# Kernel optimization log

Measured on AMD Instinct MI355X. Metric: run time of the kernel, lower is better.

The kernel has to match this reference:

```python
import jax, jax.numpy as jnp
import numpy as np

DIM = 1024
HEADS = 16


def setup_inputs() -> dict:
    key = jax.random.key(0)
    k1, k2, k3, k4 = jax.random.split(key, 4)
    x = jax.random.normal(k1, (4, 2048, DIM), dtype=jnp.float32)
    # torch nn.Linear weights: [out_features, in_features]
    w_qkv = jax.random.normal(k2, (3 * DIM, DIM), dtype=jnp.float32) * (DIM ** -0.5)
    w_out = jax.random.normal(k3, (DIM, DIM), dtype=jnp.float32) * (DIM ** -0.5)
    b_out = jax.random.normal(k4, (DIM,), dtype=jnp.float32) * 0.01
    return {"x": x, "w_qkv": w_qkv, "w_out": w_out, "b_out": b_out}


def reference(x, w_qkv, w_out, b_out):
    b, n, d = x.shape
    h = HEADS
    hd = d // h
    scale = d ** -0.5  # note: full dim, matching the original module
    qkv = jnp.einsum('bnd,ed->bne', x, w_qkv)  # [b, n, 3d]
    q, k, v = jnp.split(qkv, 3, axis=-1)
    def to_heads(t):
        return t.reshape(b, n, h, hd).transpose(0, 2, 1, 3)  # [b, h, n, hd]
    q, k, v = map(to_heads, (q, k, v))
    dots = jnp.einsum('bhqd,bhkd->bhqk', q, k) * scale  # [b, h, n, n]
    attn = jax.nn.softmax(dots, axis=-1)
    out = jnp.einsum('bhqk,bhkd->bhqd', attn, v)  # [b, h, n, hd]
    out = out.transpose(0, 2, 1, 3).reshape(b, n, d)
    return jnp.einsum('bnd,ed->bne', out, w_out) + b_out
```

## Files before the change

kernel.cpp:

```cpp
#include <hip/hip_runtime.h>
#include <stdint.h>

#define SEQ   2048
#define NDIM  1024
#define NH    16
#define HD    64
#define KDIM  1024

typedef short  short8  __attribute__((ext_vector_type(8)));
typedef float  floatx4 __attribute__((ext_vector_type(4)));
typedef unsigned short ushort4v __attribute__((ext_vector_type(4)));
typedef _Float16 half4 __attribute__((ext_vector_type(4)));
typedef __fp16  fp16x2 __attribute__((ext_vector_type(2)));
typedef __fp16  fp16x4 __attribute__((ext_vector_type(4)));

typedef __attribute__((address_space(1))) void GV;
typedef __attribute__((address_space(3))) void LV;

#define QSCALE 0.04508422003f

__device__ __forceinline__ unsigned short f2bf(float f) {
    unsigned int u = __float_as_uint(f);
    u += 0x7fffu + ((u >> 16) & 1u);
    return (unsigned short)(u >> 16);
}

__global__ __launch_bounds__(256) void cast_f32_bf16(const float* __restrict__ in,
                                                     unsigned short* __restrict__ out) {
    int i = (blockIdx.x * 256 + threadIdx.x) * 4;
    float4 v = *(const float4*)(in + i);
    ushort4v o;
    o.x = f2bf(v.x); o.y = f2bf(v.y); o.z = f2bf(v.z); o.w = f2bf(v.w);
    *(ushort4v*)(out + i) = o;
}

template<int MODE>
__global__ __launch_bounds__(256, 2)
void gemm_bt(const unsigned short* __restrict__ A,
             const unsigned short* __restrict__ B,
             unsigned short* __restrict__ Cq,
             unsigned short* __restrict__ Ck,
             unsigned short* __restrict__ Cv,
             const float* __restrict__ bias,
             float* __restrict__ Cout)
{
    __shared__ unsigned short As[128 * 32];
    __shared__ unsigned short Bs[128 * 32];
    const int tid  = threadIdx.x;
    const int lane = tid & 63;
    const int w    = tid >> 6;
    const int quad = lane >> 4;
    const int l15  = lane & 15;
    const int wm   = w >> 1, wn = w & 1;
    const int bm   = blockIdx.x, bn = blockIdx.y;

    const unsigned short* Arow = A + (size_t)bm * 128 * KDIM;
    const unsigned short* Brow = B + (size_t)bn * 128 * KDIM;

    const unsigned short* ga[2]; const unsigned short* gb[2];
    unsigned short* la[2];       unsigned short* lb[2];
#pragma unroll
    for (int i = 0; i < 2; ++i) {
        int j = ((w * 2 + i) << 6) + lane;
        int r = j >> 2;
        int c = (j & 3) ^ ((r >> 1) & 3);
        ga[i] = Arow + r * KDIM + c * 8;
        gb[i] = Brow + r * KDIM + c * 8;
        la[i] = (unsigned short*)As + ((w * 2 + i) << 9);
        lb[i] = (unsigned short*)Bs + ((w * 2 + i) << 9);
    }

    int achunk[4], bchunk[4];
#pragma unroll
    for (int t = 0; t < 4; ++t) {
        int ra = wm * 64 + t * 16 + l15;
        achunk[t] = (ra << 2) + (quad ^ ((ra >> 1) & 3));
        int rb = wn * 64 + t * 16 + l15;
        bchunk[t] = (rb << 2) + (quad ^ ((rb >> 1) & 3));
    }

    floatx4 acc[4][4];
#pragma unroll
    for (int mt = 0; mt < 4; ++mt)
#pragma unroll
        for (int nt = 0; nt < 4; ++nt)
            acc[mt][nt] = (floatx4){0.f, 0.f, 0.f, 0.f};

    for (int kt = 0; kt < KDIM / 32; ++kt) {
#pragma unroll
        for (int i = 0; i < 2; ++i) {
            __builtin_amdgcn_global_load_lds((GV*)(void*)(ga[i] + kt * 32), (LV*)(void*)la[i], 16, 0, 0);
            __builtin_amdgcn_global_load_lds((GV*)(void*)(gb[i] + kt * 32), (LV*)(void*)lb[i], 16, 0, 0);
        }
        __syncthreads();
        short8 af[4], bf[4];
#pragma unroll
        for (int t = 0; t < 4; ++t) {
            af[t] = *(const short8*)(As + (achunk[t] << 3));
            bf[t] = *(const short8*)(Bs + (bchunk[t] << 3));
        }
#pragma unroll
        for (int mt = 0; mt < 4; ++mt)
#pragma unroll
            for (int nt = 0; nt < 4; ++nt)
                acc[mt][nt] = __builtin_amdgcn_mfma_f32_16x16x32_bf16(af[mt], bf[nt], acc[mt][nt], 0, 0, 0);
        __syncthreads();
    }

    if (MODE == 0) {
        const int which = bn >> 3;
        unsigned short* dst = which == 0 ? Cq : (which == 1 ? Ck : Cv);
#pragma unroll
        for (int nt = 0; nt < 4; ++nt) {
            int e0   = ((bn & 7) << 7) + wn * 64 + nt * 16;
            int head = e0 >> 6;
            int hdi  = (e0 & 63) + l15;
#pragma unroll
            for (int mt = 0; mt < 4; ++mt) {
#pragma unroll
                for (int r = 0; r < 4; ++r) {
                    int m = bm * 128 + wm * 64 + mt * 16 + quad * 4 + r;
                    int b = m >> 11, n = m & 2047;
                    int bh = (b << 4) + head;
                    float val = acc[mt][nt][r];
                    if (which == 0) {
                        dst[((size_t)bh * SEQ + n) * HD + hdi] = f2bf(val * QSCALE);
                    } else if (which == 1) {
                        size_t idx = (size_t)bh * 131072
                                   + (size_t)(n >> 7) * 8192
                                   + (size_t)((((n >> 4) & 7) * 2) + (hdi >> 5)) * 512
                                   + ((((hdi >> 3) & 3) * 16) + (n & 15)) * 8
                                   + (hdi & 7);
                        dst[idx] = f2bf(val);
                    } else {
                        size_t idx = (size_t)bh * 131072
                                   + (size_t)(n >> 7) * 8192
                                   + (size_t)((((n >> 4) & 7) * 4) + (hdi >> 4)) * 256
                                   + ((((n >> 2) & 3) * 16) + (hdi & 15)) * 4
                                   + (n & 3);
                        _Float16 hv = (_Float16)val;
                        dst[idx] = __builtin_bit_cast(unsigned short, hv);
                    }
                }
            }
        }
    } else {
#pragma unroll
        for (int nt = 0; nt < 4; ++nt) {
            int e = bn * 128 + wn * 64 + nt * 16 + l15;
            float bv = bias[e];
#pragma unroll
            for (int mt = 0; mt < 4; ++mt) {
#pragma unroll
                for (int r = 0; r < 4; ++r) {
                    int m = bm * 128 + wm * 64 + mt * 16 + quad * 4 + r;
                    Cout[(size_t)m * NDIM + e] = acc[mt][nt][r] + bv;
                }
            }
        }
    }
}

__global__ __launch_bounds__(256, 4)
void attn_fused(const unsigned short* __restrict__ qb,
                const unsigned short* __restrict__ kfrag,
                const unsigned short* __restrict__ vfrag,
                unsigned short* __restrict__ ob)
{
    __shared__ unsigned short Ks[8192];
    __shared__ unsigned short Vs[8192];

    const int tid  = threadIdx.x;
    const int lane = tid & 63;
    const int w    = tid >> 6;
    const int quad = lane >> 4;
    const int l15  = lane & 15;

    const int bid  = blockIdx.x;
    const int xcd  = bid & 7;
    const int slot = bid >> 3;
    const int bh   = xcd * 8 + (slot >> 4);
    const int q0   = (slot & 15) * 128;

    const unsigned short* Qb = qb    + (size_t)bh * SEQ * HD;
    const unsigned short* Kb = kfrag + (size_t)bh * 131072;
    const unsigned short* Vb = vfrag + (size_t)bh * 131072;

    short8 qf[2][2];
#pragma unroll
    for (int qt = 0; qt < 2; ++qt)
#pragma unroll
        for (int ks = 0; ks < 2; ++ks)
            qf[qt][ks] = *(const short8*)(Qb + (size_t)(q0 + w * 32 + qt * 16 + l15) * HD + ks * 32 + quad * 8);

    floatx4 oacc[2][4];
    floatx4 lacc[2];
#pragma unroll
    for (int qt = 0; qt < 2; ++qt) {
#pragma unroll
        for (int nt = 0; nt < 4; ++nt) oacc[qt][nt] = (floatx4){0.f, 0.f, 0.f, 0.f};
        lacc[qt] = (floatx4){0.f, 0.f, 0.f, 0.f};
    }

    const unsigned short* gk[4]; const unsigned short* gv[4];
    unsigned short* lk[4];       unsigned short* lv[4];
#pragma unroll
    for (int i = 0; i < 4; ++i) {
        int chunk = ((w * 4 + i) << 6) + lane;
        gk[i] = Kb + chunk * 8;
        gv[i] = Vb + chunk * 8;
        lk[i] = (unsigned short*)Ks + ((w * 4 + i) << 9);
        lv[i] = (unsigned short*)Vs + ((w * 4 + i) << 9);
    }

    for (int kt = 0; kt < 16; ++kt) {
#pragma unroll
        for (int i = 0; i < 4; ++i) {
            __builtin_amdgcn_global_load_lds((GV*)(void*)(gk[i] + kt * 8192), (LV*)(void*)lk[i], 16, 0, 0);
            __builtin_amdgcn_global_load_lds((GV*)(void*)(gv[i] + kt * 8192), (LV*)(void*)lv[i], 16, 0, 0);
        }
        __syncthreads();

        floatx4 sacc[2][8];
#pragma unroll
        for (int qt = 0; qt < 2; ++qt)
#pragma unroll
            for (int nt = 0; nt < 8; ++nt) sacc[qt][nt] = (floatx4){0.f, 0.f, 0.f, 0.f};
#pragma unroll
        for (int ks = 0; ks < 2; ++ks) {
#pragma unroll
            for (int nt = 0; nt < 8; ++nt) {
                short8 kf = *(const short8*)(Ks + (nt * 2 + ks) * 512 + lane * 8);
                sacc[0][nt] = __builtin_amdgcn_mfma_f32_16x16x32_bf16(kf, qf[0][ks], sacc[0][nt], 0, 0, 0);
                sacc[1][nt] = __builtin_amdgcn_mfma_f32_16x16x32_bf16(kf, qf[1][ks], sacc[1][nt], 0, 0, 0);
            }
        }

#pragma unroll
        for (int h = 0; h < 2; ++h) {
            half4 pf[2][4];
#pragma unroll
            for (int qt = 0; qt < 2; ++qt) {
#pragma unroll
                for (int k4 = 0; k4 < 4; ++k4) {
                    floatx4 s = sacc[qt][h * 4 + k4];
                    floatx4 p;
#pragma unroll
                    for (int j = 0; j < 4; ++j) p[j] = exp2f(s[j]);
                    lacc[qt] += p;
                    fp16x2 lo = __builtin_amdgcn_cvt_pkrtz(p[0], p[1]);
                    fp16x2 hi = __builtin_amdgcn_cvt_pkrtz(p[2], p[3]);
                    fp16x4 pk;
                    pk.x = lo.x; pk.y = lo.y; pk.z = hi.x; pk.w = hi.y;
                    pf[qt][k4] = __builtin_bit_cast(half4, pk);
                }
            }
#pragma unroll
            for (int k4 = 0; k4 < 4; ++k4) {
                int ktile = h * 4 + k4;
#pragma unroll
                for (int nt = 0; nt < 4; ++nt) {
                    half4 vf = *(const half4*)((const _Float16*)Vs + (ktile * 4 + nt) * 256 + lane * 4);
                    oacc[0][nt] = __builtin_amdgcn_mfma_f32_16x16x16f16(pf[0][k4], vf, oacc[0][nt], 0, 0, 0);
                    oacc[1][nt] = __builtin_amdgcn_mfma_f32_16x16x16f16(pf[1][k4], vf, oacc[1][nt], 0, 0, 0);
                }
            }
        }
        __syncthreads();
    }

    const int b = bh >> 4, h = bh & 15;
#pragma unroll
    for (int qt = 0; qt < 2; ++qt) {
        float lr = lacc[qt][0] + lacc[qt][1] + lacc[qt][2] + lacc[qt][3];
        lr += __shfl_xor(lr, 16, 64);
        lr += __shfl_xor(lr, 32, 64);
#pragma unroll
        for (int r = 0; r < 4; ++r) {
            float lq  = __shfl(lr, quad * 4 + r, 64);
            float inv = 1.f / lq;
            int n = q0 + w * 32 + qt * 16 + quad * 4 + r;
            size_t rowoff = ((size_t)b * SEQ + n) * NDIM + h * HD;
#pragma unroll
            for (int nt = 0; nt < 4; ++nt)
                ob[rowoff + nt * 16 + l15] = f2bf(oacc[qt][nt][r] * inv);
        }
    }
}

extern "C" void kernel_launch(void* const* d_in, const int* in_sizes, int n_in,
                              void* d_out, int out_size, void* d_ws, size_t ws_size,
                              hipStream_t stream)
{
    (void)in_sizes; (void)n_in; (void)out_size; (void)ws_size;
    const float* x    = (const float*)d_in[0];
    const float* wqkv = (const float*)d_in[1];
    const float* wout = (const float*)d_in[2];
    const float* bout = (const float*)d_in[3];
    float* out = (float*)d_out;

    unsigned short* xb    = (unsigned short*)d_ws;
    unsigned short* wqkvb = xb    + 8388608;
    unsigned short* woutb = wqkvb + 3145728;
    unsigned short* qbuf  = woutb + 1048576;
    unsigned short* kbuf  = qbuf  + 8388608;
    unsigned short* vbuf  = kbuf  + 8388608;
    unsigned short* obuf  = vbuf  + 8388608;

    cast_f32_bf16<<<8192, 256, 0, stream>>>(x, xb);
    cast_f32_bf16<<<3072, 256, 0, stream>>>(wqkv, wqkvb);
    cast_f32_bf16<<<1024, 256, 0, stream>>>(wout, woutb);

    gemm_bt<0><<<dim3(64, 24), 256, 0, stream>>>(xb, wqkvb, qbuf, kbuf, vbuf, nullptr, nullptr);
    attn_fused<<<1024, 256, 0, stream>>>(qbuf, kbuf, vbuf, obuf);
    gemm_bt<1><<<dim3(64, 8), 256, 0, stream>>>(obuf, woutb, nullptr, nullptr, nullptr, bout, out);
}
```

Baseline: 309.4 us.

## Register-prefetch K/V tiles, MFMA row sums, fast exp2, wider V fragment loads

Replaces the async global-to-LDS loads with register prefetch of the next K/V tile, issued after the barrier so the global loads overlap the current tile's compute. Row-sum accumulation moves onto the matrix cores by multiplying P with a ones vector, which removes the final cross-lane shuffles. exp2f becomes the hardware exp2 builtin. The V fragment layout is reorganised so each lane reads 16 bytes covering two output tiles. GEMM launch bounds go from 2 to 3 blocks per SM; together these changes add register pressure and extra MFMA work.

```diff
diff --git a/kernel.cpp b/kernel.cpp
--- a/kernel.cpp
+++ b/kernel.cpp
@@ -12,7 +12,8 @@
 typedef unsigned short ushort4v __attribute__((ext_vector_type(4)));
 typedef _Float16 half4 __attribute__((ext_vector_type(4)));
 typedef __fp16  fp16x2 __attribute__((ext_vector_type(2)));
-typedef __fp16  fp16x4 __attribute__((ext_vector_type(4)));
+typedef unsigned int uint2v __attribute__((ext_vector_type(2)));
+typedef unsigned int uint4v __attribute__((ext_vector_type(4)));
 
 typedef __attribute__((address_space(1))) void GV;
 typedef __attribute__((address_space(3))) void LV;
@@ -23,6 +24,14 @@
     unsigned int u = __float_as_uint(f);
     u += 0x7fffu + ((u >> 16) & 1u);
     return (unsigned short)(u >> 16);
+}
+
+__device__ __forceinline__ float ex2(float x) {
+#if __has_builtin(__builtin_amdgcn_exp2f)
+    return __builtin_amdgcn_exp2f(x);
+#else
+    return exp2f(x);
+#endif
 }
 
 __global__ __launch_bounds__(256) void cast_f32_bf16(const float* __restrict__ in,
@@ -35,7 +44,7 @@
 }
 
 template<int MODE>
-__global__ __launch_bounds__(256, 2)
+__global__ __launch_bounds__(256, 3)
 void gemm_bt(const unsigned short* __restrict__ A,
              const unsigned short* __restrict__ B,
              unsigned short* __restrict__ Cq,
@@ -135,8 +144,9 @@
                     } else {
                         size_t idx = (size_t)bh * 131072
                                    + (size_t)(n >> 7) * 8192
-                                   + (size_t)((((n >> 4) & 7) * 4) + (hdi >> 4)) * 256
-                                   + ((((n >> 2) & 3) * 16) + (hdi & 15)) * 4
+                                   + (size_t)((((n >> 4) & 7) * 2) + ((hdi >> 5) & 1)) * 512
+                                   + ((((n >> 2) & 3) * 16) + (hdi & 15)) * 8
+                                   + ((hdi >> 4) & 1) * 4
                                    + (n & 3);
                         _Float16 hv = (_Float16)val;
                         dst[idx] = __builtin_bit_cast(unsigned short, hv);
@@ -194,13 +204,16 @@
             qf[qt][ks] = *(const short8*)(Qb + (size_t)(q0 + w * 32 + qt * 16 + l15) * HD + ks * 32 + quad * 8);
 
     floatx4 oacc[2][4];
-    floatx4 lacc[2];
+    floatx4 lacc4[2];
 #pragma unroll
     for (int qt = 0; qt < 2; ++qt) {
 #pragma unroll
         for (int nt = 0; nt < 4; ++nt) oacc[qt][nt] = (floatx4){0.f, 0.f, 0.f, 0.f};
-        lacc[qt] = (floatx4){0.f, 0.f, 0.f, 0.f};
-    }
+        lacc4[qt] = (floatx4){0.f, 0.f, 0.f, 0.f};
+    }
+    half4 vones;
+    vones[0] = (_Float16)1.0f; vones[1] = (_Float16)1.0f;
+    vones[2] = (_Float16)1.0f; vones[3] = (_Float16)1.0f;
 
     const unsigned short* gk[4]; const unsigned short* gv[4];
     unsigned short* lk[4];       unsigned short* lv[4];
@@ -209,17 +222,31 @@
         int chunk = ((w * 4 + i) << 6) + lane;
         gk[i] = Kb + chunk * 8;
         gv[i] = Vb + chunk * 8;
-        lk[i] = (unsigned short*)Ks + ((w * 4 + i) << 9);
-        lv[i] = (unsigned short*)Vs + ((w * 4 + i) << 9);
+        lk[i] = (unsigned short*)Ks + ((w * 4 + i) << 9) + lane * 8;
+        lv[i] = (unsigned short*)Vs + ((w * 4 + i) << 9) + lane * 8;
+    }
+
+    uint4v pk[4], pv[4];
+#pragma unroll
+    for (int i = 0; i < 4; ++i) {
+        pk[i] = *(const uint4v*)gk[i];
+        pv[i] = *(const uint4v*)gv[i];
     }
 
     for (int kt = 0; kt < 16; ++kt) {
 #pragma unroll
         for (int i = 0; i < 4; ++i) {
-            __builtin_amdgcn_global_load_lds((GV*)(void*)(gk[i] + kt * 8192), (LV*)(void*)lk[i], 16, 0, 0);
-            __builtin_amdgcn_global_load_lds((GV*)(void*)(gv[i] + kt * 8192), (LV*)(void*)lv[i], 16, 0, 0);
+            *(uint4v*)lk[i] = pk[i];
+            *(uint4v*)lv[i] = pv[i];
         }
         __syncthreads();
+        if (kt < 15) {
+#pragma unroll
+            for (int i = 0; i < 4; ++i) {
+                pk[i] = *(const uint4v*)(gk[i] + (kt + 1) * 8192);
+                pv[i] = *(const uint4v*)(gv[i] + (kt + 1) * 8192);
+            }
+        }
 
         floatx4 sacc[2][8];
 #pragma unroll
@@ -237,33 +264,31 @@
         }
 
 #pragma unroll
-        for (int h = 0; h < 2; ++h) {
-            half4 pf[2][4];
+        for (int ktile = 0; ktile < 8; ++ktile) {
+            half4 pf[2];
 #pragma unroll
             for (int qt = 0; qt < 2; ++qt) {
-#pragma unroll
-                for (int k4 = 0; k4 < 4; ++k4) {
-                    floatx4 s = sacc[qt][h * 4 + k4];
-                    floatx4 p;
-#pragma unroll
-                    for (int j = 0; j < 4; ++j) p[j] = exp2f(s[j]);
-                    lacc[qt] += p;
-                    fp16x2 lo = __builtin_amdgcn_cvt_pkrtz(p[0], p[1]);
-                    fp16x2 hi = __builtin_amdgcn_cvt_pkrtz(p[2], p[3]);
-                    fp16x4 pk;
-                    pk.x = lo.x; pk.y = lo.y; pk.z = hi.x; pk.w = hi.y;
-                    pf[qt][k4] = __builtin_bit_cast(half4, pk);
-                }
-            }
-#pragma unroll
-            for (int k4 = 0; k4 < 4; ++k4) {
-                int ktile = h * 4 + k4;
-#pragma unroll
-                for (int nt = 0; nt < 4; ++nt) {
-                    half4 vf = *(const half4*)((const _Float16*)Vs + (ktile * 4 + nt) * 256 + lane * 4);
-                    oacc[0][nt] = __builtin_amdgcn_mfma_f32_16x16x16f16(pf[0][k4], vf, oacc[0][nt], 0, 0, 0);
-                    oacc[1][nt] = __builtin_amdgcn_mfma_f32_16x16x16f16(pf[1][k4], vf, oacc[1][nt], 0, 0, 0);
-                }
+                floatx4 s = sacc[qt][ktile];
+                float p0 = ex2(s[0]), p1 = ex2(s[1]), p2 = ex2(s[2]), p3 = ex2(s[3]);
+                fp16x2 lo = __builtin_amdgcn_cvt_pkrtz(p0, p1);
+                fp16x2 hi = __builtin_amdgcn_cvt_pkrtz(p2, p3);
+                uint2v u;
+                u.x = __builtin_bit_cast(unsigned int, lo);
+                u.y = __builtin_bit_cast(unsigned int, hi);
+                pf[qt] = __builtin_bit_cast(half4, u);
+                lacc4[qt] = __builtin_amdgcn_mfma_f32_16x16x16f16(pf[qt], vones, lacc4[qt], 0, 0, 0);
+            }
+#pragma unroll
+            for (int nh = 0; nh < 2; ++nh) {
+                uint4v vv = *(const uint4v*)((const unsigned short*)Vs + (ktile * 2 + nh) * 512 + lane * 8);
+                uint2v v0; v0.x = vv.x; v0.y = vv.y;
+                uint2v v1; v1.x = vv.z; v1.y = vv.w;
+                half4 vf0 = __builtin_bit_cast(half4, v0);
+                half4 vf1 = __builtin_bit_cast(half4, v1);
+                oacc[0][nh * 2 + 0] = __builtin_amdgcn_mfma_f32_16x16x16f16(pf[0], vf0, oacc[0][nh * 2 + 0], 0, 0, 0);
+                oacc[0][nh * 2 + 1] = __builtin_amdgcn_mfma_f32_16x16x16f16(pf[0], vf1, oacc[0][nh * 2 + 1], 0, 0, 0);
+                oacc[1][nh * 2 + 0] = __builtin_amdgcn_mfma_f32_16x16x16f16(pf[1], vf0, oacc[1][nh * 2 + 0], 0, 0, 0);
+                oacc[1][nh * 2 + 1] = __builtin_amdgcn_mfma_f32_16x16x16f16(pf[1], vf1, oacc[1][nh * 2 + 1], 0, 0, 0);
             }
         }
         __syncthreads();
@@ -272,13 +297,9 @@
     const int b = bh >> 4, h = bh & 15;
 #pragma unroll
     for (int qt = 0; qt < 2; ++qt) {
-        float lr = lacc[qt][0] + lacc[qt][1] + lacc[qt][2] + lacc[qt][3];
-        lr += __shfl_xor(lr, 16, 64);
-        lr += __shfl_xor(lr, 32, 64);
 #pragma unroll
         for (int r = 0; r < 4; ++r) {
-            float lq  = __shfl(lr, quad * 4 + r, 64);
-            float inv = 1.f / lq;
+            float inv = 1.f / lacc4[qt][r];
             int n = q0 + w * 32 + qt * 16 + quad * 4 + r;
             size_t rowoff = ((size_t)b * SEQ + n) * NDIM + h * HD;
 #pragma unroll
```

Result: faster. 291.7 us (-5.7%).
